# Optimization experiments

Measured on AMD Instinct MI355X. Metric: run time of the kernel, lower is better.

## Reference

```python
import jax, jax.numpy as jnp
import numpy as np

EMBED = 1024
HEADS = 16
HEAD_DIM = EMBED // HEADS
OUT_DIM = 1024


def setup_inputs() -> dict:
    key = jax.random.key(0)
    ks = jax.random.split(key, 8)
    N, L = 2, 2048
    values = jax.random.normal(ks[0], (N, L, EMBED), dtype=jnp.float32)
    keys_t = jax.random.normal(ks[1], (N, L, EMBED), dtype=jnp.float32)
    query = jax.random.normal(ks[2], (N, L, EMBED), dtype=jnp.float32)
    s = 1.0 / np.sqrt(HEAD_DIM)
    Wv = jax.random.normal(ks[3], (HEAD_DIM, HEAD_DIM), dtype=jnp.float32) * s
    Wk = jax.random.normal(ks[4], (HEAD_DIM, HEAD_DIM), dtype=jnp.float32) * s
    Wq = jax.random.normal(ks[5], (HEAD_DIM, HEAD_DIM), dtype=jnp.float32) * s
    Wout = jax.random.normal(ks[6], (OUT_DIM, EMBED), dtype=jnp.float32) * (1.0 / np.sqrt(EMBED))
    bout = jax.random.normal(ks[7], (OUT_DIM,), dtype=jnp.float32) * 0.01
    return {"values": values, "keys": keys_t, "query": query,
            "Wv": Wv, "Wk": Wk, "Wq": Wq, "Wout": Wout, "bout": bout}


def reference(values, keys, query, Wv, Wk, Wq, Wout, bout):
    N, Lq, _ = query.shape
    Lk = keys.shape[1]
    # split into heads: (N, L, H, D)
    v = values.reshape(N, Lk, HEADS, HEAD_DIM)
    k = keys.reshape(N, Lk, HEADS, HEAD_DIM)
    q = query.reshape(N, Lq, HEADS, HEAD_DIM)
    # per-head shared linear projections (torch Linear: x @ W.T, no bias)
    v = jnp.einsum('nlhd,ed->nlhe', v, Wv)
    k = jnp.einsum('nlhd,ed->nlhe', k, Wk)
    q = jnp.einsum('nqhd,ed->nqhe', q, Wq)
    # scores (N, H, Q, K); NOTE: scale is 1/sqrt(embed_size), per original code
    scores = jnp.einsum('nqhd,nkhd->nhqk', q, k) / jnp.sqrt(jnp.float32(EMBED))
    attn = jax.nn.softmax(scores, axis=-1)
    out = jnp.einsum('nhqk,nkhd->nqhd', attn, v).reshape(N, Lq, EMBED)
    # fc_out: x @ Wout.T + bout
    return out @ Wout.T + bout
```

## Files before the change

kernel.cpp:

```cpp
#include <hip/hip_runtime.h>
#include <cstdint>

typedef __attribute__((ext_vector_type(8))) short short8;
typedef __attribute__((ext_vector_type(4))) float floatx4;
typedef __attribute__((ext_vector_type(4))) _Float16 half4;

#define DEV __device__ __forceinline__

constexpr int NB = 2, Lseq = 2048, NH = 16, HD = 64, EMB = 1024;
constexpr float QSCALE = 0.03125f * 1.4426950408889634f;

DEV uint16_t f2bf(float f) {
  uint32_t x = __builtin_bit_cast(uint32_t, f);
  x += 0x7fffu + ((x >> 16) & 1u);
  return (uint16_t)(x >> 16);
}

DEV uint32_t pack2(float lo, float hi) {
  uint32_t a = __builtin_bit_cast(uint32_t, lo) + 0x8000u;
  uint32_t b = __builtin_bit_cast(uint32_t, hi) + 0x8000u;
  return __builtin_amdgcn_perm(b, a, 0x07060302);
}

DEV uint32_t packh2(float lo, float hi) {
  return __builtin_bit_cast(uint32_t, __builtin_amdgcn_cvt_pkrtz(lo, hi));
}

DEV void gl_lds16(const void* g, void* l) {
  __builtin_amdgcn_global_load_lds((const __attribute__((address_space(1))) void*)g,
                                   (__attribute__((address_space(3))) void*)l, 16, 0, 0);
}

DEV short8 ld8bf(const float* p, float sc) {
  float4 u = *(const float4*)p;
  float4 v = *(const float4*)(p + 4);
  union { short8 s; uint32_t d[4]; } r;
  r.d[0] = pack2(u.x * sc, u.y * sc);
  r.d[1] = pack2(u.z * sc, u.w * sc);
  r.d[2] = pack2(v.x * sc, v.y * sc);
  r.d[3] = pack2(v.z * sc, v.w * sc);
  return r.s;
}

__global__ __launch_bounds__(256) void prep_kernel(
    const float* __restrict__ values, const float* __restrict__ keysrc,
    const float* __restrict__ query, const float* __restrict__ Wv,
    const float* __restrict__ Wk, const float* __restrict__ Wq,
    const float* __restrict__ Wout,
    uint16_t* __restrict__ qp, uint16_t* __restrict__ kp,
    uint16_t* __restrict__ vp, uint16_t* __restrict__ wbf) {
  const int t = threadIdx.x, w = t >> 6, lane = t & 63;
  const int quad = lane >> 4, l16 = lane & 15;
  const int wid = blockIdx.x * 4 + w;
  const int mat = wid >> 10, sub = wid & 1023;

  if (mat == 3) {
#pragma unroll
    for (int i = 0; i < 4; ++i) {
      int idx = sub * 256 + i * 64 + lane;
      float4 v = ((const float4*)Wout)[idx];
      uint2 p;
      p.x = pack2(v.x, v.y);
      p.y = pack2(v.z, v.w);
      ((uint2*)wbf)[idx] = p;
    }
    return;
  }

  floatx4 c[4][4];
#pragma unroll
  for (int i = 0; i < 4; ++i)
#pragma unroll
    for (int j = 0; j < 4; ++j) c[i][j] = floatx4{0.f, 0.f, 0.f, 0.f};

  if (mat < 2) {
    const float* src = mat ? keysrc : query;
    const float* W   = mat ? Wk : Wq;
    const float asc  = mat ? 1.f : QSCALE;
    uint16_t* dst    = mat ? kp : qp;
    const int R0 = sub * 64;
    short8 a[4][2], b[4][2];
#pragma unroll
    for (int dc = 0; dc < 2; ++dc) {
#pragma unroll
      for (int f = 0; f < 4; ++f) {
        a[f][dc] = ld8bf(W + (size_t)(f * 16 + l16) * 64 + dc * 32 + quad * 8, asc);
        b[f][dc] = ld8bf(src + (size_t)(R0 + f * 16 + l16) * 64 + dc * 32 + quad * 8, 1.f);
      }
    }
#pragma unroll
    for (int dc = 0; dc < 2; ++dc)
#pragma unroll
      for (int mf = 0; mf < 4; ++mf)
#pragma unroll
        for (int nf = 0; nf < 4; ++nf)
          c[mf][nf] = __builtin_amdgcn_mfma_f32_16x16x32_bf16(a[mf][dc], b[nf][dc], c[mf][nf], 0, 0, 0);
#pragma unroll
    for (int nf = 0; nf < 4; ++nf) {
      int r = R0 + nf * 16 + l16;
      int h = r & 15, l = (r >> 4) & 2047, n = r >> 15;
      uint16_t* drow = dst + ((size_t)(n * 16 + h) * 2048 + l) * 64;
#pragma unroll
      for (int mf = 0; mf < 4; ++mf) {
        uint2 pk;
        pk.x = pack2(c[mf][nf][0], c[mf][nf][1]);
        pk.y = pack2(c[mf][nf][2], c[mf][nf][3]);
        *(uint2*)(drow + mf * 16 + quad * 4) = pk;
      }
    }
  } else {
    const int nh = sub >> 5, L0 = (sub & 31) * 64;
    const int n = nh >> 4, h = nh & 15;
    short8 a[4][2], b[4][2];
#pragma unroll
    for (int dc = 0; dc < 2; ++dc) {
#pragma unroll
      for (int f = 0; f < 4; ++f) {
        a[f][dc] = ld8bf(values + (size_t)(n * 2048 + L0 + f * 16 + l16) * 1024 + h * 64 + dc * 32 + quad * 8, 1.f);
        b[f][dc] = ld8bf(Wv + (size_t)(f * 16 + l16) * 64 + dc * 32 + quad * 8, 1.f);
      }
    }
#pragma unroll
    for (int dc = 0; dc < 2; ++dc)
#pragma unroll
      for (int mf = 0; mf < 4; ++mf)
#pragma unroll
        for (int nf = 0; nf < 4; ++nf)
          c[mf][nf] = __builtin_amdgcn_mfma_f32_16x16x32_bf16(a[mf][dc], b[nf][dc], c[mf][nf], 0, 0, 0);
#pragma unroll
    for (int nf = 0; nf < 4; ++nf) {
      int d = nf * 16 + l16;
      uint16_t* drow = vp + ((size_t)nh * 64 + d) * 2048 + L0;
#pragma unroll
      for (int mf = 0; mf < 4; ++mf) {
        uint2 pk;
        pk.x = packh2(c[mf][nf][0], c[mf][nf][1]);
        pk.y = packh2(c[mf][nf][2], c[mf][nf][3]);
        *(uint2*)(drow + mf * 16 + quad * 4) = pk;
      }
    }
  }
}

__global__ __launch_bounds__(256, 4) void flash_kernel(const uint16_t* __restrict__ qp,
                                                       const uint16_t* __restrict__ kp,
                                                       const uint16_t* __restrict__ vp,
                                                       uint16_t* __restrict__ xatt) {
  constexpr int kbn = 32;
  __shared__ uint16_t Kt[2][64 * 64];
  __shared__ uint16_t Vt[2][64 * 64];
  const int t = threadIdx.x;
  const int w = t >> 6, lane = t & 63, quad = lane >> 4, l16 = lane & 15;
  const int nh = blockIdx.x, qt = blockIdx.y;
  const int q0 = qt * 64 + w * 16;
  const uint16_t* Qb = qp + (size_t)nh * Lseq * HD;
  const uint16_t* Kb = kp + (size_t)nh * Lseq * HD;
  const uint16_t* Vb = vp + (size_t)nh * HD * Lseq;
  const int srow = lane >> 3, sc8 = (lane & 7) ^ (lane >> 3);

  short8 bq[2];
  bq[0] = *(const short8*)(Qb + (q0 + l16) * 64 + quad * 8);
  bq[1] = *(const short8*)(Qb + (q0 + l16) * 64 + 32 + quad * 8);

  floatx4 o[4];
  floatx4 lfr;
#pragma unroll
  for (int i = 0; i < 4; ++i) o[i] = floatx4{0.f, 0.f, 0.f, 0.f};
  lfr = floatx4{0.f, 0.f, 0.f, 0.f};
  const _Float16 one = (_Float16)1.0f;
  const half4 vone = {one, one, one, one};

#pragma unroll
  for (int i = 0; i < 2; ++i) {
    int r0 = w * 16 + i * 8;
    gl_lds16(Kb + (r0 + srow) * 64 + sc8 * 8, &Kt[0][r0 * 64]);
    gl_lds16(Vb + (size_t)(r0 + srow) * Lseq + sc8 * 8, &Vt[0][r0 * 64]);
  }

  for (int kb = 0; kb < kbn; ++kb) {
    __syncthreads();
    const int cur = kb & 1;
    if (kb + 1 < kbn) {
      const int nxt = cur ^ 1;
      const uint16_t* kg = Kb + (kb + 1) * (64 * 64);
#pragma unroll
      for (int i = 0; i < 2; ++i) {
        int r0 = w * 16 + i * 8;
        gl_lds16(kg + (r0 + srow) * 64 + sc8 * 8, &Kt[nxt][r0 * 64]);
        gl_lds16(Vb + (size_t)(r0 + srow) * Lseq + (kb + 1) * 64 + sc8 * 8, &Vt[nxt][r0 * 64]);
      }
    }

    floatx4 s[4];
#pragma unroll
    for (int kb16 = 0; kb16 < 4; ++kb16) s[kb16] = floatx4{0.f, 0.f, 0.f, 0.f};
#pragma unroll
    for (int dc = 0; dc < 2; ++dc) {
#pragma unroll
      for (int kb16 = 0; kb16 < 4; ++kb16) {
        int row = kb16 * 16 + l16;
        short8 ak = *(const short8*)(&Kt[cur][row * 64 + ((dc * 4 + quad) ^ (row & 7)) * 8]);
        s[kb16] = __builtin_amdgcn_mfma_f32_16x16x32_bf16(ak, bq[dc], s[kb16], 0, 0, 0);
      }
    }

    half4 bp[4];
#pragma unroll
    for (int kb16 = 0; kb16 < 4; ++kb16) {
      float p0 = __builtin_amdgcn_exp2f(s[kb16][0]);
      float p1 = __builtin_amdgcn_exp2f(s[kb16][1]);
      float p2 = __builtin_amdgcn_exp2f(s[kb16][2]);
      float p3 = __builtin_amdgcn_exp2f(s[kb16][3]);
      union { half4 h4; uint32_t d[2]; } u;
      u.d[0] = packh2(p0, p1);
      u.d[1] = packh2(p2, p3);
      bp[kb16] = u.h4;
    }
#pragma unroll
    for (int kb16 = 0; kb16 < 4; ++kb16)
      lfr = __builtin_amdgcn_mfma_f32_16x16x16f16(vone, bp[kb16], lfr, 0, 0, 0);

#pragma unroll
    for (int kb16 = 0; kb16 < 4; ++kb16) {
#pragma unroll
      for (int db = 0; db < 4; ++db) {
        int row = db * 16 + l16;
        int ch = (kb16 * 2 + (quad >> 1)) ^ (row & 7);
        half4 av = *(const half4*)(&Vt[cur][row * 64 + ch * 8 + (quad & 1) * 4]);
        o[db] = __builtin_amdgcn_mfma_f32_16x16x16f16(av, bp[kb16], o[db], 0, 0, 0);
      }
    }
  }

  const int n = nh >> 4, h = nh & 15;
  float inv = __builtin_amdgcn_rcpf(lfr[0]);
  size_t rowb = (size_t)(n * Lseq + q0 + l16) * EMB + h * 64;
#pragma unroll
  for (int db = 0; db < 4; ++db) {
    uint2 pk;
    pk.x = pack2(o[db][0] * inv, o[db][1] * inv);
    pk.y = pack2(o[db][2] * inv, o[db][3] * inv);
    *(uint2*)(xatt + rowb + db * 16 + quad * 4) = pk;
  }
}

__global__ __launch_bounds__(256, 2) void gemm_xat(const uint16_t* __restrict__ X,
                                                   const uint16_t* __restrict__ Wb,
                                                   const float* __restrict__ bias,
                                                   float* __restrict__ out) {
  __shared__ uint16_t Xt[2][64 * 64];
  __shared__ uint16_t Wt[2][128 * 64];
  const int t = threadIdx.x, w = t >> 6, lane = t & 63, quad = lane >> 4, l16 = lane & 15;
  const int m0 = blockIdx.x * 64, o0 = blockIdx.y * 128;
  const int srow = lane >> 3, sc8 = (lane & 7) ^ (lane >> 3);

  floatx4 acc[8];
#pragma unroll
  for (int j = 0; j < 8; ++j) acc[j] = floatx4{0.f, 0.f, 0.f, 0.f};

  auto dma = [&](int buf, int kt) {
    const int e0 = kt * 64;
#pragma unroll
    for (int i = 0; i < 2; ++i) {
      int r0 = w * 16 + i * 8;
      gl_lds16(X + (size_t)(m0 + r0 + srow) * 1024 + e0 + sc8 * 8, &Xt[buf][r0 * 64]);
    }
#pragma unroll
    for (int i = 0; i < 4; ++i) {
      int r0 = w * 32 + i * 8;
      gl_lds16(Wb + (size_t)(o0 + r0 + srow) * 1024 + e0 + sc8 * 8, &Wt[buf][r0 * 64]);
    }
  };

  dma(0, 0);

  for (int kt = 0; kt < 16; ++kt) {
    const int cur = kt & 1;
    __syncthreads();
    if (kt + 1 < 16) dma(cur ^ 1, kt + 1);
#pragma unroll
    for (int kc = 0; kc < 2; ++kc) {
      int ra = w * 16 + l16;
      short8 a = *(const short8*)(&Xt[cur][ra * 64 + ((kc * 4 + quad) ^ (ra & 7)) * 8]);
#pragma unroll
      for (int nf = 0; nf < 8; ++nf) {
        int rb = nf * 16 + l16;
        short8 b = *(const short8*)(&Wt[cur][rb * 64 + ((kc * 4 + quad) ^ (rb & 7)) * 8]);
        acc[nf] = __builtin_amdgcn_mfma_f32_16x16x32_bf16(a, b, acc[nf], 0, 0, 0);
      }
    }
  }

#pragma unroll
  for (int nf = 0; nf < 8; ++nf) {
    float bv = bias[o0 + nf * 16 + l16];
#pragma unroll
    for (int r = 0; r < 4; ++r)
      out[(size_t)(m0 + w * 16 + quad * 4 + r) * 1024 + o0 + nf * 16 + l16] = acc[nf][r] + bv;
  }
}

extern "C" void kernel_launch(void* const* d_in, const int* in_sizes, int n_in,
                              void* d_out, int out_size, void* d_ws, size_t ws_size,
                              hipStream_t stream) {
  const float* values = (const float*)d_in[0];
  const float* keys   = (const float*)d_in[1];
  const float* query  = (const float*)d_in[2];
  const float* Wv     = (const float*)d_in[3];
  const float* Wk     = (const float*)d_in[4];
  const float* Wq     = (const float*)d_in[5];
  const float* Wout   = (const float*)d_in[6];
  const float* bout   = (const float*)d_in[7];
  float* out = (float*)d_out;
  (void)ws_size;

  uint16_t* ws  = (uint16_t*)d_ws;
  uint16_t* qp  = ws;
  uint16_t* kp  = ws + (size_t)4194304;
  uint16_t* vp  = ws + (size_t)8388608;
  uint16_t* wbf = ws + (size_t)12582912;
  uint16_t* xat = ws + (size_t)13631488;

  prep_kernel<<<dim3(1024), dim3(256), 0, stream>>>(values, keys, query, Wv, Wk, Wq, Wout,
                                                    qp, kp, vp, wbf);
  flash_kernel<<<dim3(32, 32), dim3(256), 0, stream>>>(qp, kp, vp, xat);
  gemm_xat<<<dim3(64, 8), dim3(256), 0, stream>>>(xat, wbf, bout, out);
}
```

Measured before the change: 180.9 us.

## Split flash attention key blocks across warps and reduce partial outputs in LDS

Each warp now handles all 64 queries of the block against its own 16-key slice of each key tile, where before each warp handled 16 queries against all 64 keys. Partial O accumulators and row sums are combined across the four warps through shared memory at the end. The aim is to share each K/V LDS fragment across four query MFMAs and cut LDS reads per MFMA. In exchange it uses many more accumulator registers, so launch bounds drop to 2 blocks per CU, and it adds an LDS reduction epilogue with extra barriers.

```diff
diff --git a/kernel.cpp b/kernel.cpp
--- a/kernel.cpp
+++ b/kernel.cpp
@@ -142,31 +142,39 @@
   }
 }
 
-__global__ __launch_bounds__(256, 4) void flash_kernel(const uint16_t* __restrict__ qp,
+__global__ __launch_bounds__(256, 2) void flash_kernel(const uint16_t* __restrict__ qp,
                                                        const uint16_t* __restrict__ kp,
                                                        const uint16_t* __restrict__ vp,
                                                        uint16_t* __restrict__ xatt) {
   constexpr int kbn = 32;
   __shared__ uint16_t Kt[2][64 * 64];
   __shared__ uint16_t Vt[2][64 * 64];
+  __shared__ float cmb[4][1024];
+  __shared__ float lfb[4][64];
   const int t = threadIdx.x;
   const int w = t >> 6, lane = t & 63, quad = lane >> 4, l16 = lane & 15;
   const int nh = blockIdx.x, qt = blockIdx.y;
-  const int q0 = qt * 64 + w * 16;
+  const int q0 = qt * 64;
   const uint16_t* Qb = qp + (size_t)nh * Lseq * HD;
   const uint16_t* Kb = kp + (size_t)nh * Lseq * HD;
   const uint16_t* Vb = vp + (size_t)nh * HD * Lseq;
   const int srow = lane >> 3, sc8 = (lane & 7) ^ (lane >> 3);
 
-  short8 bq[2];
-  bq[0] = *(const short8*)(Qb + (q0 + l16) * 64 + quad * 8);
-  bq[1] = *(const short8*)(Qb + (q0 + l16) * 64 + 32 + quad * 8);
-
-  floatx4 o[4];
-  floatx4 lfr;
-#pragma unroll
-  for (int i = 0; i < 4; ++i) o[i] = floatx4{0.f, 0.f, 0.f, 0.f};
-  lfr = floatx4{0.f, 0.f, 0.f, 0.f};
+  short8 bq[4][2];
+#pragma unroll
+  for (int qb = 0; qb < 4; ++qb) {
+    bq[qb][0] = *(const short8*)(Qb + (q0 + qb * 16 + l16) * 64 + quad * 8);
+    bq[qb][1] = *(const short8*)(Qb + (q0 + qb * 16 + l16) * 64 + 32 + quad * 8);
+  }
+
+  floatx4 o[4][4];
+  floatx4 lfr[4];
+#pragma unroll
+  for (int i = 0; i < 4; ++i) {
+    lfr[i] = floatx4{0.f, 0.f, 0.f, 0.f};
+#pragma unroll
+    for (int j = 0; j < 4; ++j) o[i][j] = floatx4{0.f, 0.f, 0.f, 0.f};
+  }
   const _Float16 one = (_Float16)1.0f;
   const half4 vone = {one, one, one, one};
 
@@ -176,6 +184,9 @@
     gl_lds16(Kb + (r0 + srow) * 64 + sc8 * 8, &Kt[0][r0 * 64]);
     gl_lds16(Vb + (size_t)(r0 + srow) * Lseq + sc8 * 8, &Vt[0][r0 * 64]);
   }
+
+  const int krow = w * 16 + l16;
+  const int kch0 = w * 2;
 
   for (int kb = 0; kb < kbn; ++kb) {
     __syncthreads();
@@ -193,54 +204,67 @@
 
     floatx4 s[4];
 #pragma unroll
-    for (int kb16 = 0; kb16 < 4; ++kb16) s[kb16] = floatx4{0.f, 0.f, 0.f, 0.f};
+    for (int qb = 0; qb < 4; ++qb) s[qb] = floatx4{0.f, 0.f, 0.f, 0.f};
 #pragma unroll
     for (int dc = 0; dc < 2; ++dc) {
-#pragma unroll
-      for (int kb16 = 0; kb16 < 4; ++kb16) {
-        int row = kb16 * 16 + l16;
-        short8 ak = *(const short8*)(&Kt[cur][row * 64 + ((dc * 4 + quad) ^ (row & 7)) * 8]);
-        s[kb16] = __builtin_amdgcn_mfma_f32_16x16x32_bf16(ak, bq[dc], s[kb16], 0, 0, 0);
-      }
+      short8 ak = *(const short8*)(&Kt[cur][krow * 64 + ((dc * 4 + quad) ^ (krow & 7)) * 8]);
+#pragma unroll
+      for (int qb = 0; qb < 4; ++qb)
+        s[qb] = __builtin_amdgcn_mfma_f32_16x16x32_bf16(ak, bq[qb][dc], s[qb], 0, 0, 0);
     }
 
     half4 bp[4];
 #pragma unroll
-    for (int kb16 = 0; kb16 < 4; ++kb16) {
-      float p0 = __builtin_amdgcn_exp2f(s[kb16][0]);
-      float p1 = __builtin_amdgcn_exp2f(s[kb16][1]);
-      float p2 = __builtin_amdgcn_exp2f(s[kb16][2]);
-      float p3 = __builtin_amdgcn_exp2f(s[kb16][3]);
+    for (int qb = 0; qb < 4; ++qb) {
+      float p0 = __builtin_amdgcn_exp2f(s[qb][0]);
+      float p1 = __builtin_amdgcn_exp2f(s[qb][1]);
+      float p2 = __builtin_amdgcn_exp2f(s[qb][2]);
+      float p3 = __builtin_amdgcn_exp2f(s[qb][3]);
       union { half4 h4; uint32_t d[2]; } u;
       u.d[0] = packh2(p0, p1);
       u.d[1] = packh2(p2, p3);
-      bp[kb16] = u.h4;
-    }
-#pragma unroll
-    for (int kb16 = 0; kb16 < 4; ++kb16)
-      lfr = __builtin_amdgcn_mfma_f32_16x16x16f16(vone, bp[kb16], lfr, 0, 0, 0);
-
-#pragma unroll
-    for (int kb16 = 0; kb16 < 4; ++kb16) {
-#pragma unroll
-      for (int db = 0; db < 4; ++db) {
-        int row = db * 16 + l16;
-        int ch = (kb16 * 2 + (quad >> 1)) ^ (row & 7);
-        half4 av = *(const half4*)(&Vt[cur][row * 64 + ch * 8 + (quad & 1) * 4]);
-        o[db] = __builtin_amdgcn_mfma_f32_16x16x16f16(av, bp[kb16], o[db], 0, 0, 0);
-      }
-    }
+      bp[qb] = u.h4;
+      lfr[qb] = __builtin_amdgcn_mfma_f32_16x16x16f16(vone, bp[qb], lfr[qb], 0, 0, 0);
+    }
+
+#pragma unroll
+    for (int db = 0; db < 4; ++db) {
+      int row = db * 16 + l16;
+      int ch = (kch0 + (quad >> 1)) ^ (row & 7);
+      half4 av = *(const half4*)(&Vt[cur][row * 64 + ch * 8 + (quad & 1) * 4]);
+#pragma unroll
+      for (int qb = 0; qb < 4; ++qb)
+        o[db][qb] = __builtin_amdgcn_mfma_f32_16x16x16f16(av, bp[qb], o[db][qb], 0, 0, 0);
+    }
+  }
+
+  if (quad == 0) {
+#pragma unroll
+    for (int qb = 0; qb < 4; ++qb) lfb[w][qb * 16 + l16] = lfr[qb][0];
   }
 
   const int n = nh >> 4, h = nh & 15;
-  float inv = __builtin_amdgcn_rcpf(lfr[0]);
-  size_t rowb = (size_t)(n * Lseq + q0 + l16) * EMB + h * 64;
+  const int cq = t >> 2, cd = (t & 3) * 4;
 #pragma unroll
   for (int db = 0; db < 4; ++db) {
+    __syncthreads();
+#pragma unroll
+    for (int qb = 0; qb < 4; ++qb)
+      *(floatx4*)(&cmb[w][(qb * 16 + l16) * 16 + quad * 4]) = o[db][qb];
+    __syncthreads();
+    floatx4 a0 = *(const floatx4*)(&cmb[0][cq * 16 + cd]);
+    floatx4 a1 = *(const floatx4*)(&cmb[1][cq * 16 + cd]);
+    floatx4 a2 = *(const floatx4*)(&cmb[2][cq * 16 + cd]);
+    floatx4 a3 = *(const floatx4*)(&cmb[3][cq * 16 + cd]);
+    float inv = __builtin_amdgcn_rcpf(lfb[0][cq] + lfb[1][cq] + lfb[2][cq] + lfb[3][cq]);
+    float v0 = (a0[0] + a1[0] + a2[0] + a3[0]) * inv;
+    float v1 = (a0[1] + a1[1] + a2[1] + a3[1]) * inv;
+    float v2 = (a0[2] + a1[2] + a2[2] + a3[2]) * inv;
+    float v3 = (a0[3] + a1[3] + a2[3] + a3[3]) * inv;
     uint2 pk;
-    pk.x = pack2(o[db][0] * inv, o[db][1] * inv);
-    pk.y = pack2(o[db][2] * inv, o[db][3] * inv);
-    *(uint2*)(xatt + rowb + db * 16 + quad * 4) = pk;
+    pk.x = pack2(v0, v1);
+    pk.y = pack2(v2, v3);
+    *(uint2*)(xatt + (size_t)(n * Lseq + q0 + cq) * EMB + h * 64 + db * 16 + cd) = pk;
   }
 }
 
```

Result: slower. 187.4 us (+3.6%).
